# Kernel optimization log

Hardware: AMD Instinct MI355X
Metric: run time of the kernel (lower is better)

The kernel has to match this reference:

```python
import jax, jax.numpy as jnp
import numpy as np

G = 5000      # n_genes (nodes)
IN = 64       # in_dim
D = 128       # embed_dims
E = 240000    # edges (before self-loops)
SLOPE = 0.2   # leakyrelu_slope (outer) and GATv2 internal negative_slope (PyG default 0.2)


def setup_inputs() -> dict:
    key = jax.random.key(0)
    ks = jax.random.split(key, 12)
    s = 0.05
    return {
        "x": jax.random.normal(ks[0], (G, IN), jnp.float32),
        "edge_index": jax.random.randint(ks[1], (2, E), 0, G, jnp.int64),
        # per-gene input linears: n_genes independent Linear(in_dim -> embed_dims)
        "W_in": jax.random.normal(ks[2], (G, IN, D), jnp.float32) * s,
        "b_in": jnp.zeros((G, D), jnp.float32),
        # GATv2Conv params (heads=1): lin_l, lin_r, att, bias
        "W_l": jax.random.normal(ks[3], (D, D), jnp.float32) * s,
        "b_l": jnp.zeros((D,), jnp.float32),
        "W_r": jax.random.normal(ks[4], (D, D), jnp.float32) * s,
        "b_r": jnp.zeros((D,), jnp.float32),
        "att": jax.random.normal(ks[5], (D,), jnp.float32) * s,
        "bias": jnp.zeros((D,), jnp.float32),
        # output MLP: Linear(D*G -> D), Linear(D -> 1)
        "W1": jax.random.normal(ks[6], (D * G, D), jnp.float32) * 0.001,
        "b1": jnp.zeros((D,), jnp.float32),
        "W2": jax.random.normal(ks[7], (D, 1), jnp.float32) * s,
        "b2": jnp.zeros((1,), jnp.float32),
    }


def _leaky(v, slope):
    return jnp.where(v >= 0, v, slope * v)


def reference(x, edge_index, W_in, b_in, W_l, b_l, W_r, b_r, att, bias, W1, b1, W2, b2):
    # per-gene linear + relu: [G, IN] x [G, IN, D] -> [G, D]
    h = jax.nn.relu(jnp.einsum("gi,gid->gd", x, W_in) + b_in)

    # GATv2Conv (heads=1, concat, add_self_loops=True)
    xl = h @ W_l + b_l  # source-side transform [G, D]
    xr = h @ W_r + b_r  # target-side transform [G, D]
    loop = jnp.arange(G, dtype=edge_index.dtype)
    src = jnp.concatenate([edge_index[0], loop])  # [E+G]
    dst = jnp.concatenate([edge_index[1], loop])

    # attention logits per edge: att . LeakyReLU(xl[src] + xr[dst])
    e = _leaky(xl[src] + xr[dst], 0.2) @ att  # [E+G]

    # segment softmax over edges sharing a destination
    m = jax.ops.segment_max(e, dst, num_segments=G)  # [G]
    w = jnp.exp(e - m[dst])
    z = jax.ops.segment_sum(w, dst, num_segments=G)  # [G]
    alpha = w / z[dst]  # every node has a self-loop, z > 0

    # scatter-aggregate weighted messages
    out = jax.ops.segment_sum(alpha[:, None] * xl[src], dst, num_segments=G) + bias  # [G, D]

    out = _leaky(out, SLOPE)
    flat = out.reshape(-1)  # [G*D]
    h1 = jax.nn.relu(flat @ W1 + b1)
    return h1 @ W2 + b2  # [1]
```

## Files before the change

### kernel.cpp

```cpp
#include <hip/hip_runtime.h>
#include <math.h>

#define G 5000
#define IN 64
#define D 128
#define E 240000
#define EG (E + G)
#define SLOPE 0.2f
#define GD (G * D)
#define CAP 128
#define NB_M 1250
#define NB_PG 1250
#define NB_H 240

__device__ __forceinline__ float leaky(float v) { return v >= 0.f ? v : SLOPE * v; }

__global__ __launch_bounds__(256) void k_fuseA(const float* __restrict__ x,
                                               const float* __restrict__ Win,
                                               const float* __restrict__ bin,
                                               const float* __restrict__ Wl,
                                               const float* __restrict__ bl,
                                               const float* __restrict__ Wr,
                                               const float* __restrict__ br,
                                               float* __restrict__ xl,
                                               float* __restrict__ xr,
                                               const int* __restrict__ srcA,
                                               const int* __restrict__ dstA,
                                               int* __restrict__ cnt,
                                               int* __restrict__ ssrc,
                                               float* __restrict__ outz) {
    if (blockIdx.x == 0 && threadIdx.x == 0) *outz = 0.f;
    if (blockIdx.x < NB_PG) {
        int g = (blockIdx.x * 256 + threadIdx.x) >> 6;
        int lane = threadIdx.x & 63;
        if (g >= G) return;
        float xv = x[g * IN + lane];
        const float* W = Win + (size_t)g * IN * D + lane * 2;
        float2 acc = *(const float2*)(bin + g * D + lane * 2);
#pragma unroll
        for (int i = 0; i < IN; ++i) {
            float xi = __shfl(xv, i);
            float2 w2 = *(const float2*)(W + (size_t)i * D);
            acc.x = fmaf(xi, w2.x, acc.x);
            acc.y = fmaf(xi, w2.y, acc.y);
        }
        float2 o = { fmaxf(acc.x, 0.f), fmaxf(acc.y, 0.f) };
        int d2 = lane * 2;
        float2 al = *(const float2*)(bl + d2);
        float2 ar = *(const float2*)(br + d2);
#pragma unroll 8
        for (int kp = 0; kp < 64; ++kp) {
            float hx = __shfl(o.x, kp);
            float hy = __shfl(o.y, kp);
            float2 wl0 = *(const float2*)(Wl + (2 * kp) * D + d2);
            float2 wl1 = *(const float2*)(Wl + (2 * kp + 1) * D + d2);
            float2 wr0 = *(const float2*)(Wr + (2 * kp) * D + d2);
            float2 wr1 = *(const float2*)(Wr + (2 * kp + 1) * D + d2);
            al.x = fmaf(hx, wl0.x, al.x); al.y = fmaf(hx, wl0.y, al.y);
            al.x = fmaf(hy, wl1.x, al.x); al.y = fmaf(hy, wl1.y, al.y);
            ar.x = fmaf(hx, wr0.x, ar.x); ar.y = fmaf(hx, wr0.y, ar.y);
            ar.x = fmaf(hy, wr1.x, ar.x); ar.y = fmaf(hy, wr1.y, ar.y);
        }
        *(float2*)(xl + (size_t)g * D + d2) = al;
        *(float2*)(xr + (size_t)g * D + d2) = ar;
    } else {
        int base = ((blockIdx.x - NB_PG) * 256 + threadIdx.x) * 4;
        if (base >= EG) return;
        if (base + 4 <= E) {
            int4 s4 = *(const int4*)(srcA + base);
            int4 d4 = *(const int4*)(dstA + base);
            int p;
            p = atomicAdd(&cnt[d4.x], 1); if (p < CAP) ssrc[d4.x * CAP + p] = s4.x;
            p = atomicAdd(&cnt[d4.y], 1); if (p < CAP) ssrc[d4.y * CAP + p] = s4.y;
            p = atomicAdd(&cnt[d4.z], 1); if (p < CAP) ssrc[d4.z * CAP + p] = s4.z;
            p = atomicAdd(&cnt[d4.w], 1); if (p < CAP) ssrc[d4.w * CAP + p] = s4.w;
        } else {
            for (int kk = 0; kk < 4; ++kk) {
                int i = base + kk;
                if (i < EG) {
                    int s, t;
                    if (i < E) { s = srcA[i]; t = dstA[i]; }
                    else { s = i - E; t = s; }
                    int p = atomicAdd(&cnt[t], 1);
                    if (p < CAP) ssrc[t * CAP + p] = s;
                }
            }
        }
    }
}

__global__ __launch_bounds__(256) void k_aggmlp(const int* __restrict__ cnt,
                                                const int* __restrict__ ssrc,
                                                const float* __restrict__ xl,
                                                const float* __restrict__ xr,
                                                const float* __restrict__ att,
                                                const float* __restrict__ bias,
                                                const float* __restrict__ W1,
                                                float* __restrict__ partials) {
    int wid = threadIdx.x >> 6;
    int lane = threadIdx.x & 63;
    int t = __builtin_amdgcn_readfirstlane(blockIdx.x * 4 + wid);
    __shared__ float w_lds[4][64];
    __shared__ int   s_lds[4][64];
    __shared__ float2 red[4][64];
    const float* xrt = xr + (size_t)t * D;
    int lane2 = lane * 2;
    int deg = cnt[t]; if (deg > CAP) deg = CAP;
    const int* srow = ssrc + t * CAP;
    float2 acc = { 0.f, 0.f };
    float z = 0.f;
    for (int base = 0; base < deg; base += 64) {
        int nv = deg - base; if (nv > 64) nv = 64;
        int mye = base + lane;
        int s = srow[mye < deg ? mye : deg - 1];
        const float* xls = xl + (size_t)s * D;
        float v0 = 0.f, v1 = 0.f;
#pragma unroll
        for (int dc = 0; dc < D; dc += 8) {
            float4 xa = *(const float4*)(xls + dc);
            float4 xb = *(const float4*)(xls + dc + 4);
            float4 ra = *(const float4*)(xrt + dc);
            float4 rb = *(const float4*)(xrt + dc + 4);
            float4 aa = *(const float4*)(att + dc);
            float4 ab = *(const float4*)(att + dc + 4);
            v0 = fmaf(aa.x, leaky(xa.x + ra.x), v0);
            v0 = fmaf(aa.y, leaky(xa.y + ra.y), v0);
            v0 = fmaf(aa.z, leaky(xa.z + ra.z), v0);
            v0 = fmaf(aa.w, leaky(xa.w + ra.w), v0);
            v1 = fmaf(ab.x, leaky(xb.x + rb.x), v1);
            v1 = fmaf(ab.y, leaky(xb.y + rb.y), v1);
            v1 = fmaf(ab.z, leaky(xb.z + rb.z), v1);
            v1 = fmaf(ab.w, leaky(xb.w + rb.w), v1);
        }
        float w = (lane < nv) ? expf(v0 + v1) : 0.f;
        z += w;
        w_lds[wid][lane] = w;
        s_lds[wid][lane] = s;
        for (int e = 0; e < nv; e += 4) {
            float4 w4 = *(const float4*)&w_lds[wid][e];
            int4   s4 = *(const int4*)&s_lds[wid][e];
            float2 l0 = *(const float2*)(xl + (size_t)s4.x * D + lane2);
            float2 l1 = *(const float2*)(xl + (size_t)s4.y * D + lane2);
            float2 l2 = *(const float2*)(xl + (size_t)s4.z * D + lane2);
            float2 l3 = *(const float2*)(xl + (size_t)s4.w * D + lane2);
            acc.x = fmaf(w4.x, l0.x, acc.x); acc.y = fmaf(w4.x, l0.y, acc.y);
            acc.x = fmaf(w4.y, l1.x, acc.x); acc.y = fmaf(w4.y, l1.y, acc.y);
            acc.x = fmaf(w4.z, l2.x, acc.x); acc.y = fmaf(w4.z, l2.y, acc.y);
            acc.x = fmaf(w4.w, l3.x, acc.x); acc.y = fmaf(w4.w, l3.y, acc.y);
        }
    }
#pragma unroll
    for (int off = 32; off; off >>= 1) z += __shfl_xor(z, off);
    float inv = 1.f / z;
    float2 bv = *(const float2*)(bias + lane2);
    float2 o = { leaky(acc.x * inv + bv.x), leaky(acc.y * inv + bv.y) };

    const float* W1p = W1 + (size_t)t * D * D + lane2;
    float2 m = { 0.f, 0.f };
#pragma unroll 8
    for (int dp = 0; dp < 64; ++dp) {
        float fx = __shfl(o.x, dp);
        float fy = __shfl(o.y, dp);
        float2 wa = *(const float2*)(W1p + (size_t)(2 * dp) * D);
        float2 wb = *(const float2*)(W1p + (size_t)(2 * dp + 1) * D);
        m.x = fmaf(fx, wa.x, m.x); m.y = fmaf(fx, wa.y, m.y);
        m.x = fmaf(fy, wb.x, m.x); m.y = fmaf(fy, wb.y, m.y);
    }
    red[wid][lane] = m;
    __syncthreads();
    if (wid == 0) {
        float2 s0 = red[0][lane], s1 = red[1][lane], s2 = red[2][lane], s3 = red[3][lane];
        float2 s = { s0.x + s1.x + s2.x + s3.x, s0.y + s1.y + s2.y + s3.y };
        *(float2*)(partials + (size_t)blockIdx.x * D + lane2) = s;
    }
}

__global__ __launch_bounds__(1024) void k_final8(const float* __restrict__ partials,
                                                 const float* __restrict__ b1,
                                                 const float* __restrict__ W2,
                                                 const float* __restrict__ b2,
                                                 float* __restrict__ out) {
    int tid = threadIdx.x;
    int rg = tid >> 4;
    int cl = tid & 15;
    int c = blockIdx.x * 16 + cl;
    float s = 0.f;
    for (int r = rg; r < NB_M; r += 64) s += partials[(size_t)r * D + c];
    __shared__ float red[64][16];
    red[rg][cl] = s;
    __syncthreads();
    if (tid < 128) {
        int cc = tid & 15, seg = tid >> 4;
        float t2 = red[seg * 8][cc];
        for (int m = 1; m < 8; ++m) t2 += red[seg * 8 + m][cc];
        red[seg * 8][cc] = t2;
    }
    __syncthreads();
    if (tid < 16) {
        float tot = 0.f;
        for (int m = 0; m < 8; ++m) tot += red[m * 8][tid];
        float h1 = fmaxf(tot + b1[blockIdx.x * 16 + tid], 0.f);
        red[0][tid] = h1 * W2[blockIdx.x * 16 + tid];
    }
    __syncthreads();
    if (tid == 0) {
        float o = 0.f;
        for (int m = 0; m < 16; ++m) o += red[0][m];
        if (blockIdx.x == 0) o += b2[0];
        atomicAdd(out, o);
    }
}

extern "C" void kernel_launch(void* const* d_in, const int* in_sizes, int n_in,
                              void* d_out, int out_size, void* d_ws, size_t ws_size,
                              hipStream_t stream) {
    const float* x    = (const float*)d_in[0];
    const int*   ei   = (const int*)d_in[1];
    const float* Win  = (const float*)d_in[2];
    const float* bin  = (const float*)d_in[3];
    const float* Wl   = (const float*)d_in[4];
    const float* bl   = (const float*)d_in[5];
    const float* Wr   = (const float*)d_in[6];
    const float* br   = (const float*)d_in[7];
    const float* att  = (const float*)d_in[8];
    const float* bias = (const float*)d_in[9];
    const float* W1   = (const float*)d_in[10];
    const float* b1   = (const float*)d_in[11];
    const float* W2   = (const float*)d_in[12];
    const float* b2   = (const float*)d_in[13];
    float* out = (float*)d_out;

    float* ws       = (float*)d_ws;
    float* xl       = ws;
    float* xr       = xl + GD;
    float* partials = xr + GD;
    int*   ssrc     = (int*)(partials + (size_t)NB_M * D);
    int*   cnt      = ssrc + (size_t)G * CAP;

    const int* srcA = ei;
    const int* dstA = ei + E;

    hipMemsetAsync(cnt, 0, G * sizeof(int), stream);
    k_fuseA<<<NB_PG + NB_H, 256, 0, stream>>>(x, Win, bin, Wl, bl, Wr, br, xl, xr,
                                              srcA, dstA, cnt, ssrc, out);
    k_aggmlp<<<NB_M, 256, 0, stream>>>(cnt, ssrc, xl, xr, att, bias, W1, partials);
    k_final8<<<8, 1024, 0, stream>>>(partials, b1, W2, b2, out);
}
```

Measured before the change: 172.2 us.

## Split xl/xr projection into separate kernel with multi-node register tiling

Moves the Wl/Wr projection out of the per-gene kernel, which now only writes h to a new workspace buffer. A new kernel computes xl and xr for four nodes per block, so each weight load is reused across four nodes instead of being reloaded per node with shuffles. The aim is less weight traffic and less shuffle overhead in the projection. In exchange it adds a kernel launch and an extra write and read of h through global memory.

```diff
diff --git a/kernel.cpp b/kernel.cpp
--- a/kernel.cpp
+++ b/kernel.cpp
@@ -12,18 +12,14 @@
 #define NB_M 1250
 #define NB_PG 1250
 #define NB_H 240
+#define NB_X 1250
 
 __device__ __forceinline__ float leaky(float v) { return v >= 0.f ? v : SLOPE * v; }
 
 __global__ __launch_bounds__(256) void k_fuseA(const float* __restrict__ x,
                                                const float* __restrict__ Win,
                                                const float* __restrict__ bin,
-                                               const float* __restrict__ Wl,
-                                               const float* __restrict__ bl,
-                                               const float* __restrict__ Wr,
-                                               const float* __restrict__ br,
-                                               float* __restrict__ xl,
-                                               float* __restrict__ xr,
+                                               float* __restrict__ h,
                                                const int* __restrict__ srcA,
                                                const int* __restrict__ dstA,
                                                int* __restrict__ cnt,
@@ -45,24 +41,7 @@
             acc.y = fmaf(xi, w2.y, acc.y);
         }
         float2 o = { fmaxf(acc.x, 0.f), fmaxf(acc.y, 0.f) };
-        int d2 = lane * 2;
-        float2 al = *(const float2*)(bl + d2);
-        float2 ar = *(const float2*)(br + d2);
-#pragma unroll 8
-        for (int kp = 0; kp < 64; ++kp) {
-            float hx = __shfl(o.x, kp);
-            float hy = __shfl(o.y, kp);
-            float2 wl0 = *(const float2*)(Wl + (2 * kp) * D + d2);
-            float2 wl1 = *(const float2*)(Wl + (2 * kp + 1) * D + d2);
-            float2 wr0 = *(const float2*)(Wr + (2 * kp) * D + d2);
-            float2 wr1 = *(const float2*)(Wr + (2 * kp + 1) * D + d2);
-            al.x = fmaf(hx, wl0.x, al.x); al.y = fmaf(hx, wl0.y, al.y);
-            al.x = fmaf(hy, wl1.x, al.x); al.y = fmaf(hy, wl1.y, al.y);
-            ar.x = fmaf(hx, wr0.x, ar.x); ar.y = fmaf(hx, wr0.y, ar.y);
-            ar.x = fmaf(hy, wr1.x, ar.x); ar.y = fmaf(hy, wr1.y, ar.y);
-        }
-        *(float2*)(xl + (size_t)g * D + d2) = al;
-        *(float2*)(xr + (size_t)g * D + d2) = ar;
+        *(float2*)(h + g * D + lane * 2) = o;
     } else {
         int base = ((blockIdx.x - NB_PG) * 256 + threadIdx.x) * 4;
         if (base >= EG) return;
@@ -87,6 +66,52 @@
             }
         }
     }
+}
+
+__global__ __launch_bounds__(256) void k_xlxr3(const float* __restrict__ h,
+                                               const float* __restrict__ Wl,
+                                               const float* __restrict__ bl,
+                                               const float* __restrict__ Wr,
+                                               const float* __restrict__ br,
+                                               float* __restrict__ xl,
+                                               float* __restrict__ xr) {
+    int g0 = blockIdx.x * 4;
+    int tid = threadIdx.x;
+    int half = tid >> 7;
+    int col = tid & 127;
+    const float* W = half ? Wr : Wl;
+    const float* bb = half ? br : bl;
+    float* o = half ? xr : xl;
+    const float* h0p = h + (size_t)(g0 + 0) * D;
+    const float* h1p = h + (size_t)(g0 + 1) * D;
+    const float* h2p = h + (size_t)(g0 + 2) * D;
+    const float* h3p = h + (size_t)(g0 + 3) * D;
+    float b = bb[col];
+    float acc0 = b, acc1 = b, acc2 = b, acc3 = b;
+#pragma unroll 8
+    for (int k4 = 0; k4 < 32; ++k4) {
+        int k = k4 * 4;
+        float4 hv0 = *(const float4*)(h0p + k);
+        float4 hv1 = *(const float4*)(h1p + k);
+        float4 hv2 = *(const float4*)(h2p + k);
+        float4 hv3 = *(const float4*)(h3p + k);
+        float w0 = W[(size_t)(k + 0) * D + col];
+        float w1 = W[(size_t)(k + 1) * D + col];
+        float w2 = W[(size_t)(k + 2) * D + col];
+        float w3 = W[(size_t)(k + 3) * D + col];
+        acc0 = fmaf(hv0.x, w0, acc0); acc0 = fmaf(hv0.y, w1, acc0);
+        acc0 = fmaf(hv0.z, w2, acc0); acc0 = fmaf(hv0.w, w3, acc0);
+        acc1 = fmaf(hv1.x, w0, acc1); acc1 = fmaf(hv1.y, w1, acc1);
+        acc1 = fmaf(hv1.z, w2, acc1); acc1 = fmaf(hv1.w, w3, acc1);
+        acc2 = fmaf(hv2.x, w0, acc2); acc2 = fmaf(hv2.y, w1, acc2);
+        acc2 = fmaf(hv2.z, w2, acc2); acc2 = fmaf(hv2.w, w3, acc2);
+        acc3 = fmaf(hv3.x, w0, acc3); acc3 = fmaf(hv3.y, w1, acc3);
+        acc3 = fmaf(hv3.z, w2, acc3); acc3 = fmaf(hv3.w, w3, acc3);
+    }
+    o[(size_t)(g0 + 0) * D + col] = acc0;
+    o[(size_t)(g0 + 1) * D + col] = acc1;
+    o[(size_t)(g0 + 2) * D + col] = acc2;
+    o[(size_t)(g0 + 3) * D + col] = acc3;
 }
 
 __global__ __launch_bounds__(256) void k_aggmlp(const int* __restrict__ cnt,
@@ -231,7 +256,8 @@
     float* out = (float*)d_out;
 
     float* ws       = (float*)d_ws;
-    float* xl       = ws;
+    float* h        = ws;
+    float* xl       = h  + GD;
     float* xr       = xl + GD;
     float* partials = xr + GD;
     int*   ssrc     = (int*)(partials + (size_t)NB_M * D);
@@ -241,8 +267,8 @@
     const int* dstA = ei + E;
 
     hipMemsetAsync(cnt, 0, G * sizeof(int), stream);
-    k_fuseA<<<NB_PG + NB_H, 256, 0, stream>>>(x, Win, bin, Wl, bl, Wr, br, xl, xr,
-                                              srcA, dstA, cnt, ssrc, out);
+    k_fuseA<<<NB_PG + NB_H, 256, 0, stream>>>(x, Win, bin, h, srcA, dstA, cnt, ssrc, out);
+    k_xlxr3<<<NB_X, 256, 0, stream>>>(h, Wl, bl, Wr, br, xl, xr);
     k_aggmlp<<<NB_M, 256, 0, stream>>>(cnt, ssrc, xl, xr, att, bias, W1, partials);
     k_final8<<<8, 1024, 0, stream>>>(partials, b1, W2, b2, out);
 }
```

New measurement: 154.8 us. -10.1%, faster.
